# Performance work log

Measured on AMD Instinct MI355X. Metric: run time of the kernel, lower is better.

Reference implementation:

```python
import jax, jax.numpy as jnp
import numpy as np

D_MODEL = 1024
D_FF = 4096
BATCH = 4
SEQ = 4096
DILATION = 1


def _dw_causal_conv(x, w, dilation):
    # x: [B, S, D], w: [D, 1, K] (depthwise, torch Conv1d groups=D layout)
    k = w.shape[-1]
    pad = (k - 1) * dilation
    h = jnp.transpose(x, (0, 2, 1))  # [B, D, S]
    out = jax.lax.conv_general_dilated(
        h, w,
        window_strides=(1,),
        padding=[(pad, 0)],  # causal left pad
        rhs_dilation=(dilation,),
        dimension_numbers=('NCH', 'OIH', 'NCH'),
        feature_group_count=h.shape[1],
    )
    return jnp.transpose(out, (0, 2, 1))  # [B, S, D]


def _rmsnorm(x, w):
    ms = jnp.mean(jnp.square(x), axis=-1, keepdims=True)
    return x * jax.lax.rsqrt(ms + 1e-6) * w


def setup_inputs() -> dict:
    key = jax.random.key(0)
    ks = jax.random.split(key, 12)
    s = lambda d: 1.0 / np.sqrt(d)
    return {
        'x': jax.random.normal(ks[0], (BATCH, SEQ, D_MODEL), jnp.float32),
        'ln1_w': jnp.ones((D_MODEL,), jnp.float32),
        'ln2_w': jnp.ones((D_MODEL,), jnp.float32),
        'w_fine': jax.random.normal(ks[1], (D_MODEL, 1, 3), jnp.float32) * 0.5,
        'w_medium': jax.random.normal(ks[2], (D_MODEL, 1, 5), jnp.float32) * 0.4,
        'w_coarse': jax.random.normal(ks[3], (D_MODEL, 1, 7), jnp.float32) * 0.3,
        'sg_w': jax.random.normal(ks[4], (3, D_MODEL), jnp.float32) * 0.02,
        'up_w': jax.random.normal(ks[5], (2 * D_MODEL, D_MODEL), jnp.float32) * s(D_MODEL),
        'down_w': jax.random.normal(ks[6], (D_MODEL, D_MODEL), jnp.float32) * s(D_MODEL),
        'wg': jax.random.normal(ks[7], (D_FF, D_MODEL), jnp.float32) * s(D_MODEL),
        'wu': jax.random.normal(ks[8], (D_FF, D_MODEL), jnp.float32) * s(D_MODEL),
        'wo': jax.random.normal(ks[9], (D_MODEL, D_FF), jnp.float32) * s(D_FF),
    }


def reference(x, ln1_w, ln2_w, w_fine, w_medium, w_coarse, sg_w, up_w, down_w, wg, wu, wo):
    # --- MSAC mixer with pre-norm residual ---
    h = _rmsnorm(x, ln1_w)
    gv = jnp.einsum('bsd,ed->bse', h, up_w)        # [B, S, 2D]
    gate, val = jnp.split(gv, 2, axis=-1)
    gate = jax.nn.sigmoid(gate)
    c_fine = _dw_causal_conv(val, w_fine, DILATION)
    c_medium = _dw_causal_conv(val, w_medium, DILATION)
    c_coarse = _dw_causal_conv(val, w_coarse, DILATION)
    scale_w = jax.nn.softmax(jnp.einsum('bsd,ed->bse', h, sg_w), axis=-1)  # [B, S, 3]
    fused = (scale_w[..., 0:1] * c_fine
             + scale_w[..., 1:2] * c_medium
             + scale_w[..., 2:3] * c_coarse)
    x = x + jnp.einsum('bsd,ed->bse', fused * gate, down_w)
    # --- SwiGLU FFN with pre-norm residual ---
    h2 = _rmsnorm(x, ln2_w)
    g = jax.nn.silu(jnp.einsum('bsd,fd->bsf', h2, wg))
    u = jnp.einsum('bsd,fd->bsf', h2, wu)
    x = x + jnp.einsum('bsf,df->bsd', g * u, wo)
    return x
```

## Files before the change

kernel.cpp:

```cpp
#include <hip/hip_runtime.h>
#include <stdint.h>

#define D_MODEL 1024
#define D_FF    4096
#define NTOK    16384
#define SEQ     4096

typedef __bf16 bf16x8 __attribute__((ext_vector_type(8)));
typedef float  f32x4  __attribute__((ext_vector_type(4)));

typedef __attribute__((address_space(1))) void gvoid;
typedef __attribute__((address_space(3))) void svoid;

__device__ __forceinline__ unsigned short f2bf(float f) {
  union { float f; uint32_t u; } v; v.f = f;
  uint32_t u = v.u;
  u += 0x7FFFu + ((u >> 16) & 1u);
  return (unsigned short)(u >> 16);
}
__device__ __forceinline__ float bf2f(unsigned short h) {
  union { uint32_t u; float f; } v; v.u = ((uint32_t)h) << 16;
  return v.f;
}

__device__ __forceinline__ void gload16(const void* g, void* l) {
  __builtin_amdgcn_global_load_lds((gvoid*)g, (svoid*)l, 16, 0, 0);
}

__device__ __forceinline__ float fast_sigmoid(float x) {
  return __builtin_amdgcn_rcpf(1.f + __expf(-x));
}

__global__ __launch_bounds__(256) void cvt_k(const float* __restrict__ S,
                                             unsigned short* __restrict__ D, int n4) {
  int i = blockIdx.x * 256 + threadIdx.x;
  if (i < n4) {
    float4 f = reinterpret_cast<const float4*>(S)[i];
    ushort4 o;
    o.x = f2bf(f.x); o.y = f2bf(f.y); o.z = f2bf(f.z); o.w = f2bf(f.w);
    reinterpret_cast<ushort4*>(D)[i] = o;
  }
}

__global__ __launch_bounds__(256) void cvt_il_k(const float* __restrict__ G,
                                                const float* __restrict__ U,
                                                unsigned short* __restrict__ D) {
  int i = blockIdx.x * 256 + threadIdx.x;
  const int row = i >> 8;
  const int c4  = i & 255;
  const int gi = row >> 5, w = row & 31;
  const float* src = (w < 16 ? G + (size_t)(gi * 16 + w) * 1024
                             : U + (size_t)(gi * 16 + (w - 16)) * 1024) + c4 * 4;
  float4 f = *reinterpret_cast<const float4*>(src);
  ushort4 o;
  o.x = f2bf(f.x); o.y = f2bf(f.y); o.z = f2bf(f.z); o.w = f2bf(f.w);
  reinterpret_cast<ushort4*>(D)[i] = o;
}

template<bool SG>
__global__ __launch_bounds__(256) void rmsnorm_k(
    const float* __restrict__ X, const float* __restrict__ W,
    const float* __restrict__ SGW,
    unsigned short* __restrict__ H, float* __restrict__ SCL)
{
  const int n = blockIdx.x;
  const int t = threadIdx.x;
  float4 x = reinterpret_cast<const float4*>(X + (size_t)n * D_MODEL)[t];
  float4 w = reinterpret_cast<const float4*>(W)[t];
  float4 hw;
  hw.x = x.x * w.x; hw.y = x.y * w.y; hw.z = x.z * w.z; hw.w = x.w * w.w;
  float ss = x.x*x.x + x.y*x.y + x.z*x.z + x.w*x.w;
  float p0 = 0.f, p1 = 0.f, p2 = 0.f;
  if (SG) {
    float4 s0 = reinterpret_cast<const float4*>(SGW)[t];
    float4 s1 = reinterpret_cast<const float4*>(SGW + D_MODEL)[t];
    float4 s2 = reinterpret_cast<const float4*>(SGW + 2 * D_MODEL)[t];
    p0 = hw.x*s0.x + hw.y*s0.y + hw.z*s0.z + hw.w*s0.w;
    p1 = hw.x*s1.x + hw.y*s1.y + hw.z*s1.z + hw.w*s1.w;
    p2 = hw.x*s2.x + hw.y*s2.y + hw.z*s2.z + hw.w*s2.w;
  }
  #pragma unroll
  for (int off = 32; off > 0; off >>= 1) {
    ss += __shfl_xor(ss, off);
    if (SG) {
      p0 += __shfl_xor(p0, off);
      p1 += __shfl_xor(p1, off);
      p2 += __shfl_xor(p2, off);
    }
  }
  __shared__ float red[4][4];
  const int wid = t >> 6;
  if ((t & 63) == 0) { red[wid][0] = ss; red[wid][1] = p0; red[wid][2] = p1; red[wid][3] = p2; }
  __syncthreads();
  ss = red[0][0] + red[1][0] + red[2][0] + red[3][0];
  const float r = rsqrtf(ss * (1.0f / D_MODEL) + 1e-6f);
  ushort4 h4;
  h4.x = f2bf(hw.x * r); h4.y = f2bf(hw.y * r); h4.z = f2bf(hw.z * r); h4.w = f2bf(hw.w * r);
  reinterpret_cast<ushort4*>(H + (size_t)n * D_MODEL)[t] = h4;
  if (SG && t == 0) {
    float l0 = (red[0][1] + red[1][1] + red[2][1] + red[3][1]) * r;
    float l1 = (red[0][2] + red[1][2] + red[2][2] + red[3][2]) * r;
    float l2 = (red[0][3] + red[1][3] + red[2][3] + red[3][3]) * r;
    float mx = fmaxf(l0, fmaxf(l1, l2));
    float e0 = expf(l0 - mx), e1 = expf(l1 - mx), e2 = expf(l2 - mx);
    float inv = 1.f / (e0 + e1 + e2);
    SCL[n * 3 + 0] = e0 * inv; SCL[n * 3 + 1] = e1 * inv; SCL[n * 3 + 2] = e2 * inv;
  }
}

__global__ __launch_bounds__(256) void conv_k(
    const unsigned short* __restrict__ GV,
    const float* __restrict__ SCL,
    const float* __restrict__ W3, const float* __restrict__ W5, const float* __restrict__ W7,
    unsigned short* __restrict__ Y)
{
  const int n = blockIdx.x;
  const int t = threadIdx.x;
  const int d0 = t * 4;
  const int s = n & (SEQ - 1);
  const unsigned short* vbase = GV + (size_t)n * (2 * D_MODEL) + D_MODEL + d0;
  float v[7][4];
  #pragma unroll
  for (int j = 0; j < 7; ++j) {
    const int tap = 6 - j;
    if (tap <= s) {
      ushort4 u = *reinterpret_cast<const ushort4*>(vbase - (size_t)tap * (2 * D_MODEL));
      v[j][0] = bf2f(u.x); v[j][1] = bf2f(u.y); v[j][2] = bf2f(u.z); v[j][3] = bf2f(u.w);
    } else {
      v[j][0] = 0.f; v[j][1] = 0.f; v[j][2] = 0.f; v[j][3] = 0.f;
    }
  }
  ushort4 gb = *reinterpret_cast<const ushort4*>(GV + (size_t)n * (2 * D_MODEL) + d0);
  float gf[4] = { bf2f(gb.x), bf2f(gb.y), bf2f(gb.z), bf2f(gb.w) };
  const float sc0 = SCL[n * 3 + 0], sc1 = SCL[n * 3 + 1], sc2 = SCL[n * 3 + 2];
  ushort4 out;
  unsigned short o[4];
  #pragma unroll
  for (int i = 0; i < 4; ++i) {
    const int d = d0 + i;
    float c3 = W3[d*3+0]*v[4][i] + W3[d*3+1]*v[5][i] + W3[d*3+2]*v[6][i];
    float c5 = W5[d*5+0]*v[2][i] + W5[d*5+1]*v[3][i] + W5[d*5+2]*v[4][i]
             + W5[d*5+3]*v[5][i] + W5[d*5+4]*v[6][i];
    float c7 = 0.f;
    #pragma unroll
    for (int j = 0; j < 7; ++j) c7 += W7[d*7+j] * v[j][i];
    const float g = fast_sigmoid(gf[i]);
    o[i] = f2bf((sc0 * c3 + sc1 * c5 + sc2 * c7) * g);
  }
  out.x = o[0]; out.y = o[1]; out.z = o[2]; out.w = o[3];
  reinterpret_cast<ushort4*>(Y + (size_t)n * D_MODEL)[t] = out;
}


#define EPI_BF16      0
#define EPI_RES       1
#define EPI_SWIGLU_IL 2

#define STAGE_A(tt, h) do { \
    char* d_ = dstBase + (((tt)&1) << 16) + ((h) << 14); \
    const unsigned short* s_ = aSrc + (size_t)((h)*128) * K + (tt)*64; \
    gload16(s_, d_); gload16(s_ + (size_t)64 * K, d_ + 8192); } while(0)

#define STAGE_B(tt, h) do { \
    char* d_ = dstBase + (((tt)&1) << 16) + 32768 + ((h) << 14); \
    const unsigned short* s_ = bSrc + (size_t)((h)*32) * K + (tt)*64; \
    gload16(s_, d_); gload16(s_ + (size_t)128 * K, d_ + 8192); } while(0)

#define DSR(dst, base, IMM) \
  asm volatile("ds_read_b128 %0, %1 offset:" #IMM : "=v"(dst) : "v"(base))

#define RD_B0(S) do { \
  DSR(b0[0][0], bB##S##k0, 0);    DSR(b0[0][1], bB##S##k1, 0); \
  DSR(b0[1][0], bB##S##k0, 2048); DSR(b0[1][1], bB##S##k1, 2048); } while(0)

#define RD_B1(S) do { \
  DSR(b1[0][0], bB##S##k0, 16384); DSR(b1[0][1], bB##S##k1, 16384); \
  DSR(b1[1][0], bB##S##k0, 18432); DSR(b1[1][1], bB##S##k1, 18432); } while(0)

#define RD_AQ0(S) do { \
  DSR(aq[0][0], aA##S##k0, 0);    DSR(aq[0][1], aA##S##k1, 0); \
  DSR(aq[1][0], aA##S##k0, 2048); DSR(aq[1][1], aA##S##k1, 2048); \
  DSR(aq[2][0], aA##S##k0, 4096); DSR(aq[2][1], aA##S##k1, 4096); \
  DSR(aq[3][0], aA##S##k0, 6144); DSR(aq[3][1], aA##S##k1, 6144); } while(0)

#define RD_AQ1A(S) do { \
  DSR(aq[0][0], aA##S##k0, 8192);  DSR(aq[0][1], aA##S##k1, 8192); \
  DSR(aq[1][0], aA##S##k0, 10240); DSR(aq[1][1], aA##S##k1, 10240); } while(0)

#define RD_AQ1B(S) do { \
  DSR(aq[2][0], aA##S##k0, 12288); DSR(aq[2][1], aA##S##k1, 12288); \
  DSR(aq[3][0], aA##S##k0, 14336); DSR(aq[3][1], aA##S##k1, 14336); } while(0)

#define MMAQ(BR, MQ, NQ) do { \
  _Pragma("unroll") for (int f_ = 0; f_ < 4; ++f_) \
  _Pragma("unroll") for (int e_ = 0; e_ < 2; ++e_) { \
    acc[(MQ)*4+f_][(NQ)*2+e_] = __builtin_amdgcn_mfma_f32_16x16x32_bf16( \
        aq[f_][0], BR[e_][0], acc[(MQ)*4+f_][(NQ)*2+e_], 0, 0, 0); \
    acc[(MQ)*4+f_][(NQ)*2+e_] = __builtin_amdgcn_mfma_f32_16x16x32_bf16( \
        aq[f_][1], BR[e_][1], acc[(MQ)*4+f_][(NQ)*2+e_], 0, 0, 0); \
  } } while(0)

#define MMAQH(BR, MQ, NQ, F0) do { \
  _Pragma("unroll") for (int f_ = (F0); f_ < (F0) + 2; ++f_) \
  _Pragma("unroll") for (int e_ = 0; e_ < 2; ++e_) { \
    acc[(MQ)*4+f_][(NQ)*2+e_] = __builtin_amdgcn_mfma_f32_16x16x32_bf16( \
        aq[f_][0], BR[e_][0], acc[(MQ)*4+f_][(NQ)*2+e_], 0, 0, 0); \
    acc[(MQ)*4+f_][(NQ)*2+e_] = __builtin_amdgcn_mfma_f32_16x16x32_bf16( \
        aq[f_][1], BR[e_][1], acc[(MQ)*4+f_][(NQ)*2+e_], 0, 0, 0); \
  } } while(0)

#define GATE4 do { asm volatile("s_waitcnt lgkmcnt(4)" ::: "memory"); \
                   __builtin_amdgcn_sched_barrier(0); } while(0)
#define GATE0 do { asm volatile("s_waitcnt lgkmcnt(0)" ::: "memory"); \
                   __builtin_amdgcn_sched_barrier(0); } while(0)
#define VM4   asm volatile("s_waitcnt vmcnt(4)" ::: "memory")
#define VM0   asm volatile("s_waitcnt vmcnt(0)" ::: "memory")
#define BAR   __builtin_amdgcn_s_barrier()
#define PRIO1 __builtin_amdgcn_s_setprio(1)
#define PRIO0 __builtin_amdgcn_s_setprio(0)

template<int EPI>
__global__ __launch_bounds__(512, 2) void gemm256_k(
    const unsigned short* __restrict__ A,
    const unsigned short* __restrict__ B0g,
    const float* __restrict__ RES,
    void* __restrict__ OUT,
    int M, int N, int K)
{
  __shared__ uint4 lds4[8192];
  char* lbase = (char*)lds4;

  const int tid  = threadIdx.x;
  const int lane = tid & 63;
  const int wid  = tid >> 6;
  const int wm   = wid >> 2;
  const int wn   = wid & 3;
  const int l15 = lane & 15, l4 = lane >> 4, l7 = lane & 7;

  const int nbx = gridDim.x;
  const int id  = blockIdx.y * nbx + blockIdx.x;
  const int cpx = (nbx * gridDim.y) >> 3;
  const int swz = (id & 7) * cpx + (id >> 3);
  const int m0 = (swz % nbx) * 256;
  const int n0 = (swz / nbx) * 256;
  const int nt = K >> 6;

  const int r0 = tid >> 3;
  const int kc = (tid & 7) ^ (r0 & 7);
  const unsigned short* aSrc = A + (size_t)(m0 + r0) * K + kc * 8;
  const unsigned short* bSrc = B0g + (size_t)(n0 + (r0 >> 5) * 64 + (r0 & 31)) * K + kc * 8;
  char* dstBase = lbase + tid * 16;

  const unsigned colswz = (unsigned)((l4 ^ l7) << 4);
  const unsigned aA0k0 = (unsigned)((wm << 14) + l15 * 128) + colswz;
  const unsigned aA0k1 = aA0k0 ^ 0x40u;
  const unsigned aA1k0 = aA0k0 + 65536u;
  const unsigned aA1k1 = aA0k1 + 65536u;
  const unsigned bB0k0 = (unsigned)(32768 + (wn * 32 + l15) * 128) + colswz;
  const unsigned bB0k1 = bB0k0 ^ 0x40u;
  const unsigned bB1k0 = bB0k0 + 65536u;
  const unsigned bB1k1 = bB0k1 + 65536u;

  f32x4 acc[8][4];
  #pragma unroll
  for (int i = 0; i < 8; ++i)
    #pragma unroll
    for (int j = 0; j < 4; ++j)
      #pragma unroll
      for (int r = 0; r < 4; ++r) acc[i][j][r] = 0.f;

  bf16x8 aq[4][2], b0[2][2], b1[2][2];

  STAGE_A(0, 0); STAGE_A(0, 1); STAGE_B(0, 0); STAGE_B(0, 1);
  STAGE_B(1, 0); STAGE_B(1, 1);
  VM4;
  BAR;

  for (int t = 0; t + 2 < nt; t += 2) {
    RD_B0(0); RD_AQ0(0); RD_B1(0);
    STAGE_A(t + 1, 0); STAGE_A(t + 1, 1);
    GATE4; PRIO1; MMAQ(b0, 0, 0); PRIO0;
    GATE0; PRIO1; MMAQ(b1, 0, 1); PRIO0;
    BAR;
    RD_AQ1A(0); RD_AQ1B(0);
    STAGE_B(t + 2, 0); STAGE_B(t + 2, 1);
    GATE4; PRIO1; MMAQH(b1, 1, 1, 0); MMAQH(b0, 1, 0, 0); PRIO0;
    GATE0; PRIO1; MMAQH(b1, 1, 1, 2); MMAQH(b0, 1, 0, 2); PRIO0;
    VM4;
    BAR;
    RD_B0(1); RD_AQ0(1); RD_B1(1);
    STAGE_A(t + 2, 0); STAGE_A(t + 2, 1);
    GATE4; PRIO1; MMAQ(b0, 0, 0); PRIO0;
    GATE0; PRIO1; MMAQ(b1, 0, 1); PRIO0;
    BAR;
    RD_AQ1A(1); RD_AQ1B(1);
    STAGE_B(t + 3, 0); STAGE_B(t + 3, 1);
    GATE4; PRIO1; MMAQH(b1, 1, 1, 0); MMAQH(b0, 1, 0, 0); PRIO0;
    GATE0; PRIO1; MMAQH(b1, 1, 1, 2); MMAQH(b0, 1, 0, 2); PRIO0;
    VM4;
    BAR;
  }

  {
    RD_B0(0); RD_AQ0(0); RD_B1(0);
    STAGE_A(nt - 1, 0); STAGE_A(nt - 1, 1);
    GATE4; PRIO1; MMAQ(b0, 0, 0); PRIO0;
    GATE0; PRIO1; MMAQ(b1, 0, 1); PRIO0;
    BAR;
    RD_AQ1A(0); RD_AQ1B(0);
    GATE4; PRIO1; MMAQH(b1, 1, 1, 0); MMAQH(b0, 1, 0, 0); PRIO0;
    GATE0; PRIO1; MMAQH(b1, 1, 1, 2); MMAQH(b0, 1, 0, 2); PRIO0;
    VM0;
    BAR;
    RD_B0(1); RD_AQ0(1); RD_B1(1);
    GATE4; PRIO1; MMAQ(b0, 0, 0); PRIO0;
    GATE0; PRIO1; MMAQ(b1, 0, 1); PRIO0;
    BAR;
    RD_AQ1A(1); RD_AQ1B(1);
    GATE4; PRIO1; MMAQH(b1, 1, 1, 0); MMAQH(b0, 1, 0, 0); PRIO0;
    GATE0; PRIO1; MMAQH(b1, 1, 1, 2); MMAQH(b0, 1, 0, 2); PRIO0;
    BAR;
  }

  if (M < -1) ((float*)OUT)[tid] = ((float*)lds4)[tid];

  const int cr = (lane >> 4) * 4;
  const int cc = lane & 15;
  if (EPI == EPI_SWIGLU_IL) {
    const int ffbase = (n0 + wn * 64) >> 1;
    #pragma unroll
    for (int F = 0; F < 8; ++F)
      #pragma unroll
      for (int p = 0; p < 2; ++p)
        #pragma unroll
        for (int rr = 0; rr < 4; ++rr) {
          const int grow = m0 + wm * 128 + (F >> 2) * 64 + (F & 3) * 16 + cr + rr;
          const float g = acc[F][2 * p][rr];
          const float u = acc[F][2 * p + 1][rr];
          const float o = g * fast_sigmoid(g) * u;
          ((unsigned short*)OUT)[(size_t)grow * D_FF + ffbase + p * 16 + cc] = f2bf(o);
        }
  } else {
    #pragma unroll
    for (int F = 0; F < 8; ++F)
      #pragma unroll
      for (int E = 0; E < 4; ++E)
        #pragma unroll
        for (int rr = 0; rr < 4; ++rr) {
          const int grow = m0 + wm * 128 + (F >> 2) * 64 + (F & 3) * 16 + cr + rr;
          const int gcol = n0 + wn * 64 + (E >> 1) * 32 + (E & 1) * 16 + cc;
          const float v = acc[F][E][rr];
          if (EPI == EPI_BF16) {
            ((unsigned short*)OUT)[(size_t)grow * N + gcol] = f2bf(v);
          } else {
            const size_t idx = (size_t)grow * N + gcol;
            ((float*)OUT)[idx] = RES[idx] + v;
          }
        }
  }
}

extern "C" void kernel_launch(void* const* d_in, const int* in_sizes, int n_in,
                              void* d_out, int out_size, void* d_ws, size_t ws_size,
                              hipStream_t stream)
{
  const float* x    = (const float*)d_in[0];
  const float* ln1w = (const float*)d_in[1];
  const float* ln2w = (const float*)d_in[2];
  const float* wf   = (const float*)d_in[3];
  const float* wm   = (const float*)d_in[4];
  const float* wco  = (const float*)d_in[5];
  const float* sgw  = (const float*)d_in[6];
  const float* upw  = (const float*)d_in[7];
  const float* dnw  = (const float*)d_in[8];
  const float* wg   = (const float*)d_in[9];
  const float* wu   = (const float*)d_in[10];
  const float* wo   = (const float*)d_in[11];

  char* ws = (char*)d_ws;
  size_t off = 0;
  auto alloc = [&](size_t bytes) -> void* {
    void* p = ws + off;
    off += (bytes + 255) & ~(size_t)255;
    return p;
  };
  unsigned short* wb_up = (unsigned short*)alloc((size_t)2048 * 1024 * 2);
  unsigned short* wb_dn = (unsigned short*)alloc((size_t)1024 * 1024 * 2);
  unsigned short* wb_il = (unsigned short*)alloc((size_t)8192 * 1024 * 2);
  unsigned short* wb_wo = (unsigned short*)alloc((size_t)1024 * 4096 * 2);
  float*          scl   = (float*)alloc((size_t)NTOK * 3 * 4);
  unsigned short* h2b   = (unsigned short*)alloc((size_t)NTOK * D_MODEL * 2);
  char* big = (char*)alloc((size_t)NTOK * 4096 * 2);
  unsigned short* hb  = (unsigned short*)big;
  unsigned short* gvb = (unsigned short*)(big + (size_t)NTOK * 1024 * 2);
  unsigned short* yb  = (unsigned short*)(big + (size_t)NTOK * 3072 * 2);
  unsigned short* gub = (unsigned short*)big;
  float* x1 = (float*)d_out;

  cvt_k<<<2048, 256, 0, stream>>>(upw, wb_up, 2048 * 1024 / 4);
  cvt_k<<<1024, 256, 0, stream>>>(dnw, wb_dn, 1024 * 1024 / 4);
  cvt_il_k<<<8192, 256, 0, stream>>>(wg, wu, wb_il);
  cvt_k<<<4096, 256, 0, stream>>>(wo, wb_wo, 1024 * 4096 / 4);

  rmsnorm_k<true><<<NTOK, 256, 0, stream>>>(x, ln1w, sgw, hb, scl);
  gemm256_k<EPI_BF16><<<dim3(64, 8), 512, 0, stream>>>(hb, wb_up, nullptr, gvb, NTOK, 2048, 1024);
  conv_k<<<NTOK, 256, 0, stream>>>(gvb, scl, wf, wm, wco, yb);
  gemm256_k<EPI_RES><<<dim3(64, 4), 512, 0, stream>>>(yb, wb_dn, x, x1, NTOK, 1024, 1024);
  rmsnorm_k<false><<<NTOK, 256, 0, stream>>>(x1, ln2w, nullptr, h2b, nullptr);
  gemm256_k<EPI_SWIGLU_IL><<<dim3(64, 32), 512, 0, stream>>>(h2b, wb_il, nullptr, gub, NTOK, 8192, 1024);
  gemm256_k<EPI_RES><<<dim3(64, 4), 512, 0, stream>>>(gub, wb_wo, x1, (float*)d_out, NTOK, 1024, 4096);
}
```

Before: 683.9 us.

## Fuse weight conversions, drop block swizzle, issue global loads before LDS reads

Merges the four weight fp32-to-bf16 conversion kernels into one launch to cut launch overhead. Removes the grouped block-index swizzle in the GEMM, so tiles are mapped directly from blockIdx. Moves the asynchronous global-to-LDS staging loads ahead of the LDS fragment reads in each half-iteration so memory traffic starts earlier. Losing the swizzle may reduce L2 locality, and the reordering changes how memory and LDS traffic interleave.

```diff
diff --git a/kernel.cpp b/kernel.cpp
--- a/kernel.cpp
+++ b/kernel.cpp
@@ -31,30 +31,36 @@
   return __builtin_amdgcn_rcpf(1.f + __expf(-x));
 }
 
-__global__ __launch_bounds__(256) void cvt_k(const float* __restrict__ S,
-                                             unsigned short* __restrict__ D, int n4) {
-  int i = blockIdx.x * 256 + threadIdx.x;
-  if (i < n4) {
-    float4 f = reinterpret_cast<const float4*>(S)[i];
-    ushort4 o;
-    o.x = f2bf(f.x); o.y = f2bf(f.y); o.z = f2bf(f.z); o.w = f2bf(f.w);
-    reinterpret_cast<ushort4*>(D)[i] = o;
-  }
-}
-
-__global__ __launch_bounds__(256) void cvt_il_k(const float* __restrict__ G,
-                                                const float* __restrict__ U,
-                                                unsigned short* __restrict__ D) {
-  int i = blockIdx.x * 256 + threadIdx.x;
-  const int row = i >> 8;
-  const int c4  = i & 255;
-  const int gi = row >> 5, w = row & 31;
-  const float* src = (w < 16 ? G + (size_t)(gi * 16 + w) * 1024
-                             : U + (size_t)(gi * 16 + (w - 16)) * 1024) + c4 * 4;
+__global__ __launch_bounds__(256) void cvt_all_k(
+    const float* __restrict__ up, const float* __restrict__ dn,
+    const float* __restrict__ wo, const float* __restrict__ wg,
+    const float* __restrict__ wu,
+    unsigned short* __restrict__ d_up, unsigned short* __restrict__ d_dn,
+    unsigned short* __restrict__ d_wo, unsigned short* __restrict__ d_il)
+{
+  const int i = blockIdx.x * 256 + threadIdx.x;
+  const float* src;
+  unsigned short* dst;
+  if (i < 524288) {
+    src = up + (size_t)i * 4;            dst = d_up + (size_t)i * 4;
+  } else if (i < 786432) {
+    const int j = i - 524288;
+    src = dn + (size_t)j * 4;            dst = d_dn + (size_t)j * 4;
+  } else if (i < 1835008) {
+    const int j = i - 786432;
+    src = wo + (size_t)j * 4;            dst = d_wo + (size_t)j * 4;
+  } else {
+    const int j = i - 1835008;
+    const int row = j >> 8, c4 = j & 255;
+    const int gi = row >> 5, w = row & 31;
+    src = (w < 16 ? wg + (size_t)(gi * 16 + w) * 1024
+                  : wu + (size_t)(gi * 16 + (w - 16)) * 1024) + c4 * 4;
+    dst = d_il + (size_t)j * 4;
+  }
   float4 f = *reinterpret_cast<const float4*>(src);
   ushort4 o;
   o.x = f2bf(f.x); o.y = f2bf(f.y); o.z = f2bf(f.z); o.w = f2bf(f.w);
-  reinterpret_cast<ushort4*>(D)[i] = o;
+  *reinterpret_cast<ushort4*>(dst) = o;
 }
 
 template<bool SG>
@@ -236,13 +242,8 @@
   const int wm   = wid >> 2;
   const int wn   = wid & 3;
   const int l15 = lane & 15, l4 = lane >> 4, l7 = lane & 7;
-
-  const int nbx = gridDim.x;
-  const int id  = blockIdx.y * nbx + blockIdx.x;
-  const int cpx = (nbx * gridDim.y) >> 3;
-  const int swz = (id & 7) * cpx + (id >> 3);
-  const int m0 = (swz % nbx) * 256;
-  const int n0 = (swz / nbx) * 256;
+  const int m0 = blockIdx.x * 256;
+  const int n0 = blockIdx.y * 256;
   const int nt = K >> 6;
 
   const int r0 = tid >> 3;
@@ -277,24 +278,24 @@
   BAR;
 
   for (int t = 0; t + 2 < nt; t += 2) {
+    STAGE_A(t + 1, 0); STAGE_A(t + 1, 1);
     RD_B0(0); RD_AQ0(0); RD_B1(0);
-    STAGE_A(t + 1, 0); STAGE_A(t + 1, 1);
     GATE4; PRIO1; MMAQ(b0, 0, 0); PRIO0;
     GATE0; PRIO1; MMAQ(b1, 0, 1); PRIO0;
     BAR;
+    STAGE_B(t + 2, 0); STAGE_B(t + 2, 1);
     RD_AQ1A(0); RD_AQ1B(0);
-    STAGE_B(t + 2, 0); STAGE_B(t + 2, 1);
     GATE4; PRIO1; MMAQH(b1, 1, 1, 0); MMAQH(b0, 1, 0, 0); PRIO0;
     GATE0; PRIO1; MMAQH(b1, 1, 1, 2); MMAQH(b0, 1, 0, 2); PRIO0;
     VM4;
     BAR;
+    STAGE_A(t + 2, 0); STAGE_A(t + 2, 1);
     RD_B0(1); RD_AQ0(1); RD_B1(1);
-    STAGE_A(t + 2, 0); STAGE_A(t + 2, 1);
     GATE4; PRIO1; MMAQ(b0, 0, 0); PRIO0;
     GATE0; PRIO1; MMAQ(b1, 0, 1); PRIO0;
     BAR;
+    STAGE_B(t + 3, 0); STAGE_B(t + 3, 1);
     RD_AQ1A(1); RD_AQ1B(1);
-    STAGE_B(t + 3, 0); STAGE_B(t + 3, 1);
     GATE4; PRIO1; MMAQH(b1, 1, 1, 0); MMAQH(b0, 1, 0, 0); PRIO0;
     GATE0; PRIO1; MMAQH(b1, 1, 1, 2); MMAQH(b0, 1, 0, 2); PRIO0;
     VM4;
@@ -302,8 +303,8 @@
   }
 
   {
+    STAGE_A(nt - 1, 0); STAGE_A(nt - 1, 1);
     RD_B0(0); RD_AQ0(0); RD_B1(0);
-    STAGE_A(nt - 1, 0); STAGE_A(nt - 1, 1);
     GATE4; PRIO1; MMAQ(b0, 0, 0); PRIO0;
     GATE0; PRIO1; MMAQ(b1, 0, 1); PRIO0;
     BAR;
@@ -397,10 +398,8 @@
   unsigned short* gub = (unsigned short*)big;
   float* x1 = (float*)d_out;
 
-  cvt_k<<<2048, 256, 0, stream>>>(upw, wb_up, 2048 * 1024 / 4);
-  cvt_k<<<1024, 256, 0, stream>>>(dnw, wb_dn, 1024 * 1024 / 4);
-  cvt_il_k<<<8192, 256, 0, stream>>>(wg, wu, wb_il);
-  cvt_k<<<4096, 256, 0, stream>>>(wo, wb_wo, 1024 * 4096 / 4);
+  cvt_all_k<<<15360, 256, 0, stream>>>(upw, dnw, wo, wg, wu,
+                                       wb_up, wb_dn, wb_wo, wb_il);
 
   rmsnorm_k<true><<<NTOK, 256, 0, stream>>>(x, ln1w, sgw, hb, scl);
   gemm256_k<EPI_BF16><<<dim3(64, 8), 512, 0, stream>>>(hb, wb_up, nullptr, gvb, NTOK, 2048, 1024);
```

New measurement: 659.9 us (median of 2 runs). -3.5%, faster.
